# Kernel tuning notes

Hardware: AMD Instinct MI355X
Metric: run time of the kernel (lower is better)

## Reference

```python
import jax, jax.numpy as jnp
import numpy as np

C = 1.0                      # curvature
PHI = 3.1415926 * 0.3        # Cosine phase (bias=False path)
ALPHA = 0.2                  # LeakyReLU negative slope
A_PARA = 0.5                 # a_para_GATLayer
EPS = 4e-3                   # float32 ball-projection epsilon (standard HGCN)
MIN_NORM = 1e-15
NEG_INF = -9e15              # matches -9000000000000000.0 in source


def project(x, c):
    # clamp points to lie inside the Poincare ball of curvature c
    norm = jnp.maximum(jnp.linalg.norm(x, axis=-1, keepdims=True), MIN_NORM)
    maxnorm = (1.0 - EPS) / jnp.sqrt(c)
    return jnp.where(norm > maxnorm, x / norm * maxnorm, x)


def artanh(x):
    return jnp.arctanh(jnp.clip(x, -1.0 + 1e-7, 1.0 - 1e-7))


def logmap0(p, c):
    # log map at the origin of the Poincare ball
    sqrt_c = c ** 0.5
    p_norm = jnp.maximum(jnp.linalg.norm(p, axis=-1, keepdims=True), MIN_NORM)
    return artanh(sqrt_c * p_norm) / (sqrt_c * p_norm) * p


def setup_inputs() -> dict:
    key = jax.random.key(0)
    k1, k2, k3, k4 = jax.random.split(key, 4)
    N, FIN, FOUT = 8192, 512, 128
    h = jax.random.normal(k1, (N, FIN), dtype=jnp.float32)
    adj = jax.random.randint(k2, (N, N), 0, 2, dtype=jnp.int32)
    # xavier_uniform with gain=1.414
    lim_w = 1.414 * np.sqrt(6.0 / (FIN + FOUT))
    W = jax.random.uniform(k3, (FIN, FOUT), jnp.float32, -lim_w, lim_w)
    lim_a = 1.414 * np.sqrt(6.0 / (2 * FOUT + 1))
    a = jax.random.uniform(k4, (2 * FOUT, 1), jnp.float32, -lim_a, lim_a)
    return {"h": h, "adj": adj, "W": W, "a": a}


def reference(h, adj, W, a):
    fout = W.shape[1]
    Wh = h @ W                                   # [N, F_out]
    Wh1 = Wh @ a[:fout]                          # [N, 1] source score
    Wh2 = Wh @ a[fout:]                          # [N, 1] target score
    e = jax.nn.leaky_relu(Wh1 + Wh2.T, ALPHA)    # [N, N]
    e = jnp.where(adj > 0, e, NEG_INF)
    attention = jax.nn.softmax(e, axis=1)        # dropout p=0 (eval): identity
    h_prime = attention @ Wh                     # [N, F_out]
    h_prime = logmap0(project(h_prime, C), C)
    # concat=True branch: ELU + a_para * A*cos(x + phi), A=1 (data_dim=-1)
    return jax.nn.elu(h_prime) + A_PARA * jnp.cos(h_prime + PHI)
```

## Files before the change

kernel.cpp:

```cpp
#include <hip/hip_runtime.h>
#include <hip/hip_bf16.h>
#include <math.h>

typedef short short8 __attribute__((ext_vector_type(8)));
typedef float f32x4 __attribute__((ext_vector_type(4)));

static constexpr int N = 8192;
static constexpr int FIN = 512;
static constexpr int FOUT = 128;
static constexpr int NJC = 16;
static constexpr float PHI = 3.1415926f * 0.3f;
static constexpr float A_PARA = 0.5f;
static constexpr float EPS_BALL = 4e-3f;
static constexpr float L2E = 1.4426950408889634f;

__device__ __forceinline__ unsigned short f2b(float f) {
    union { float f; unsigned u; } v; v.f = f;
    unsigned r = v.u + 0x7fffu + ((v.u >> 16) & 1u);
    return (unsigned short)(r >> 16);
}

__device__ __forceinline__ short f2bn(float f) {
    __hip_bfloat16 h = __float2bfloat16(f);
    return *reinterpret_cast<short*>(&h);
}

__device__ __forceinline__ unsigned f2key(float x) {
    unsigned b = __float_as_uint(x);
    return (b & 0x80000000u) ? ~b : (b | 0x80000000u);
}
__device__ __forceinline__ float key2f(unsigned k) {
    unsigned b = (k & 0x80000000u) ? (k ^ 0x80000000u) : ~k;
    return __uint_as_float(b);
}

__device__ __forceinline__ short8 cvt8(float4 x0, float4 x1) {
    short8 r;
    r[0] = (short)f2b(x0.x); r[1] = (short)f2b(x0.y);
    r[2] = (short)f2b(x0.z); r[3] = (short)f2b(x0.w);
    r[4] = (short)f2b(x1.x); r[5] = (short)f2b(x1.y);
    r[6] = (short)f2b(x1.z); r[7] = (short)f2b(x1.w);
    return r;
}

__device__ __forceinline__ void cw(float* w, const int4 a, const float4 tv,
                                   float sA, float mA) {
    float z;
    z = sA + tv.x; w[0] = a.x > 0 ? __builtin_amdgcn_exp2f(fmaxf(z, 0.2f * z) - mA) : 0.f;
    z = sA + tv.y; w[1] = a.y > 0 ? __builtin_amdgcn_exp2f(fmaxf(z, 0.2f * z) - mA) : 0.f;
    z = sA + tv.z; w[2] = a.z > 0 ? __builtin_amdgcn_exp2f(fmaxf(z, 0.2f * z) - mA) : 0.f;
    z = sA + tv.w; w[3] = a.w > 0 ? __builtin_amdgcn_exp2f(fmaxf(z, 0.2f * z) - mA) : 0.f;
}

__global__ __launch_bounds__(256) void k0_wt(const float* __restrict__ W,
                                             unsigned short* __restrict__ Wt,
                                             unsigned* __restrict__ Tkey,
                                             float* __restrict__ denb) {
    __shared__ float sh[32][33];
    const int t = threadIdx.x;
    const int k0 = (blockIdx.x >> 2) * 32, c0 = (blockIdx.x & 3) * 32;
    {
        int r = t >> 3, c4 = (t & 7) * 4;
        float4 v = *(const float4*)(W + (size_t)(k0 + r) * FOUT + c0 + c4);
        sh[r][c4] = v.x; sh[r][c4 + 1] = v.y; sh[r][c4 + 2] = v.z; sh[r][c4 + 3] = v.w;
    }
    __syncthreads();
    int cc = t >> 3, k4 = (t & 7) * 4;
    ushort4 o;
    o.x = f2b(sh[k4][cc]); o.y = f2b(sh[k4 + 1][cc]);
    o.z = f2b(sh[k4 + 2][cc]); o.w = f2b(sh[k4 + 3][cc]);
    *(ushort4*)(Wt + (size_t)(c0 + cc) * FIN + k0 + k4) = o;
    if (blockIdx.x == 0) {
        if (t == 0) Tkey[0] = 0u;
        for (int i = t; i < N; i += 256) denb[i] = 0.f;
    }
}

__global__ __launch_bounds__(256) void k1_gemm(
    const float* __restrict__ h, const unsigned short* __restrict__ Wt,
    const float* __restrict__ a, unsigned short* __restrict__ whbt,
    float* __restrict__ s_out, float* __restrict__ t_out,
    unsigned* __restrict__ Tkey)
{
    __shared__ unsigned short hsb[2][32][72];
    __shared__ float sred[32][2], tred[32][2];
    const int t = threadIdx.x, lane = t & 63, wave = t >> 6;
    const int i0 = blockIdx.x * 32;
    const int wr = wave & 1, wc = wave >> 1;
    const int arow = lane & 15, g = lane >> 4;
    const int sr = t >> 3, sc = (t & 7) * 8;
    const float* hp = h + (size_t)(i0 + sr) * FIN + sc;

    float4 x0 = *(const float4*)hp, x1 = *(const float4*)(hp + 4);
    *(short8*)&hsb[0][sr][sc] = cvt8(x0, x1);
    __syncthreads();

    f32x4 acc[4];
    const f32x4 zz = {0.f, 0.f, 0.f, 0.f};
    #pragma unroll
    for (int cf = 0; cf < 4; ++cf) acc[cf] = zz;

    #pragma unroll 1
    for (int kt = 0; kt < 8; ++kt) {
        const int cur = kt & 1;
        float4 y0, y1;
        if (kt < 7) {
            y0 = *(const float4*)(hp + (kt + 1) * 64);
            y1 = *(const float4*)(hp + (kt + 1) * 64 + 4);
        }
        #pragma unroll
        for (int js = 0; js < 64; js += 32) {
            short8 af = *(const short8*)&hsb[cur][wr * 16 + arow][js + g * 8];
            #pragma unroll
            for (int cf = 0; cf < 4; ++cf) {
                const unsigned short* bp =
                    Wt + (size_t)(wc * 64 + cf * 16 + arow) * FIN + kt * 64 + js + g * 8;
                short8 bf = *(const short8*)bp;
                acc[cf] = __builtin_amdgcn_mfma_f32_16x16x32_bf16(af, bf, acc[cf], 0, 0, 0);
            }
        }
        if (kt < 7) {
            *(short8*)&hsb[cur ^ 1][sr][sc] = cvt8(y0, y1);
            __syncthreads();
        }
    }

    float a1v[4], a2v[4];
    #pragma unroll
    for (int cf = 0; cf < 4; ++cf) {
        int col = wc * 64 + cf * 16 + arow;
        a1v[cf] = a[col]; a2v[cf] = a[FOUT + col];
    }
    #pragma unroll
    for (int cf = 0; cf < 4; ++cf) {
        int col = wc * 64 + cf * 16 + arow;
        ushort4 o;
        o.x = f2b(acc[cf][0]); o.y = f2b(acc[cf][1]);
        o.z = f2b(acc[cf][2]); o.w = f2b(acc[cf][3]);
        *(ushort4*)(whbt + (size_t)col * N + i0 + wr * 16 + g * 4) = o;
    }
    #pragma unroll
    for (int q = 0; q < 4; ++q) {
        float sp = acc[0][q]*a1v[0] + acc[1][q]*a1v[1] + acc[2][q]*a1v[2] + acc[3][q]*a1v[3];
        float tp = acc[0][q]*a2v[0] + acc[1][q]*a2v[1] + acc[2][q]*a2v[2] + acc[3][q]*a2v[3];
        #pragma unroll
        for (int m = 1; m < 16; m <<= 1) {
            sp += __shfl_xor(sp, m, 16);
            tp += __shfl_xor(tp, m, 16);
        }
        if (arow == 0) {
            sred[wr * 16 + g * 4 + q][wc] = sp;
            tred[wr * 16 + g * 4 + q][wc] = tp;
        }
    }
    __syncthreads();
    if (t < 32) {
        float sp = (sred[t][0] + sred[t][1]) * L2E;
        float tp = (tred[t][0] + tred[t][1]) * L2E;
        s_out[i0 + t] = sp;
        t_out[i0 + t] = tp;
        float m = tp;
        #pragma unroll
        for (int d = 1; d < 32; d <<= 1) m = fmaxf(m, __shfl_xor(m, d, 32));
        if (t == 0) atomicMax(Tkey, f2key(m));
    }
}

__global__ __launch_bounds__(512, 4) void k3_attn(
    const int* __restrict__ adj, const unsigned short* __restrict__ whbt,
    const float* __restrict__ s_in, const float* __restrict__ t_in,
    const unsigned* __restrict__ Tkey,
    unsigned short* __restrict__ num_bf, float* __restrict__ num_f32,
    float* __restrict__ den_out, int slice_mode)
{
    __shared__ unsigned short bt[2][128][72];
    __shared__ float tl[512];
    const int t = threadIdx.x, lane = t & 63, wave = t >> 6;
    const int jc = blockIdx.x & (NJC - 1), it = blockIdx.x / NJC;
    const int i0 = it * 128, jbase = jc * (N / NJC);

    tl[t] = t_in[jbase + t];

    const int arow = lane & 15, g = lane >> 4;
    const int grow = i0 + wave * 16 + arow;
    const float sA = s_in[grow];
    const float Tv = key2f(Tkey[0]);
    const float zT = sA + Tv;
    const float mA = fmaxf(zT, 0.2f * zT);
    const int* adjrow = adj + (size_t)grow * N;
    const int srow = t >> 2, scol = (t & 3) * 16;
    const unsigned short* sbase = whbt + (size_t)srow * N + jbase + scol;

    f32x4 acc[8];
    const f32x4 zz = {0.f, 0.f, 0.f, 0.f};
    #pragma unroll
    for (int c = 0; c < 8; ++c) acc[c] = zz;
    float den = 0.f;

    short8 sr0 = *(const short8*)sbase;
    short8 sr1 = *(const short8*)(sbase + 8);
    int4 av0 = *(const int4*)(adjrow + jbase + g * 8);
    int4 av1 = *(const int4*)(adjrow + jbase + g * 8 + 4);
    int4 av2 = *(const int4*)(adjrow + jbase + 32 + g * 8);
    int4 av3 = *(const int4*)(adjrow + jbase + 32 + g * 8 + 4);
    *(short8*)&bt[0][srow][scol]     = sr0;
    *(short8*)&bt[0][srow][scol + 8] = sr1;
    __syncthreads();

    #pragma unroll 1
    for (int jt = 0; jt < 8; ++jt) {
        const int cur = jt & 1, jl = jt * 64;
        short8 n0, n1;
        if (jt < 7) {
            const unsigned short* p = sbase + (jt + 1) * 64;
            n0 = *(const short8*)p;
            n1 = *(const short8*)(p + 8);
        }
        int4 an0, an1, an2, an3;
        if (jt < 7) {
            const int* ap = adjrow + jbase + jl + 64;
            an0 = *(const int4*)(ap + g * 8);
            an1 = *(const int4*)(ap + g * 8 + 4);
            an2 = *(const int4*)(ap + 32 + g * 8);
            an3 = *(const int4*)(ap + 32 + g * 8 + 4);
        }
        float4 ta = *(const float4*)&tl[jl + g * 8];
        float4 tb = *(const float4*)&tl[jl + g * 8 + 4];
        float4 tc = *(const float4*)&tl[jl + 32 + g * 8];
        float4 td = *(const float4*)&tl[jl + 32 + g * 8 + 4];
        float w[16];
        cw(&w[0],  av0, ta, sA, mA);
        cw(&w[4],  av1, tb, sA, mA);
        cw(&w[8],  av2, tc, sA, mA);
        cw(&w[12], av3, td, sA, mA);
        #pragma unroll
        for (int e = 0; e < 16; ++e) den += w[e];
        short8 af0, af1;
        #pragma unroll
        for (int e = 0; e < 8; ++e) {
            af0[e] = f2bn(w[e]);
            af1[e] = f2bn(w[8 + e]);
        }
        #pragma unroll
        for (int c = 0; c < 8; ++c) {
            short8 bf = *(const short8*)&bt[cur][c * 16 + arow][g * 8];
            acc[c] = __builtin_amdgcn_mfma_f32_16x16x32_bf16(af0, bf, acc[c], 0, 0, 0);
        }
        #pragma unroll
        for (int c = 0; c < 8; ++c) {
            short8 bf = *(const short8*)&bt[cur][c * 16 + arow][32 + g * 8];
            acc[c] = __builtin_amdgcn_mfma_f32_16x16x32_bf16(af1, bf, acc[c], 0, 0, 0);
        }
        if (jt < 7) {
            *(short8*)&bt[cur ^ 1][srow][scol]     = n0;
            *(short8*)&bt[cur ^ 1][srow][scol + 8] = n1;
            av0 = an0; av1 = an1; av2 = an2; av3 = an3;
            __syncthreads();
        }
    }

    den += __shfl_xor(den, 16, 64);
    den += __shfl_xor(den, 32, 64);
    if (g == 0) atomicAdd(&den_out[grow], den);

    const int orow0 = i0 + wave * 16;
    if (slice_mode) {
        unsigned short* dst = num_bf + (size_t)jc * ((size_t)N * FOUT);
        #pragma unroll
        for (int c = 0; c < 8; ++c)
            #pragma unroll
            for (int q = 0; q < 4; ++q)
                dst[(size_t)(orow0 + g * 4 + q) * FOUT + c * 16 + arow] = f2b(acc[c][q]);
    } else {
        #pragma unroll
        for (int c = 0; c < 8; ++c)
            #pragma unroll
            for (int q = 0; q < 4; ++q)
                atomicAdd(&num_f32[(size_t)(orow0 + g * 4 + q) * FOUT + c * 16 + arow], acc[c][q]);
    }
}

__global__ __launch_bounds__(256) void k4_epi(
    const unsigned short* __restrict__ numb, const float* __restrict__ numf,
    const float* __restrict__ den, float* __restrict__ out, int bfmode)
{
    const int row = blockIdx.x * 16 + (threadIdx.x >> 4);
    const int col0 = (threadIdx.x & 15) * 8;
    const float inv = 1.0f / den[row];
    float v[8] = {};
    if (bfmode) {
        #pragma unroll 1
        for (int s5 = 0; s5 < NJC; ++s5) {
            short8 b = *(const short8*)(numb + (size_t)s5 * N * FOUT + (size_t)row * FOUT + col0);
            #pragma unroll
            for (int c = 0; c < 8; ++c)
                v[c] += __uint_as_float(((unsigned)(unsigned short)b[c]) << 16);
        }
    } else {
        #pragma unroll
        for (int c = 0; c < 8; ++c) v[c] = numf[(size_t)row * FOUT + col0 + c];
    }
    float ss = 0.f;
    #pragma unroll
    for (int c = 0; c < 8; ++c) { v[c] *= inv; ss += v[c] * v[c]; }
    #pragma unroll
    for (int m = 1; m < 16; m <<= 1) ss += __shfl_xor(ss, m, 16);
    float nrm = sqrtf(ss);
    const float maxn = 1.0f - EPS_BALL;
    float scale1 = nrm > maxn ? maxn / nrm : 1.0f;
    float pn = fminf(nrm, maxn);
    float fac;
    if (pn < 1e-6f) fac = scale1;
    else fac = scale1 * (0.5f * __logf((1.f + pn) / (1.f - pn))) / pn;
    float o[8];
    #pragma unroll
    for (int c = 0; c < 8; ++c) {
        float hv = v[c] * fac;
        float eluv = hv > 0.f ? hv : __expf(hv) - 1.f;
        o[c] = eluv + A_PARA * __cosf(hv + PHI);
    }
    float* op = out + (size_t)row * FOUT + col0;
    *(float4*)op = make_float4(o[0], o[1], o[2], o[3]);
    *(float4*)(op + 4) = make_float4(o[4], o[5], o[6], o[7]);
}

extern "C" void kernel_launch(void* const* d_in, const int* in_sizes, int n_in,
                              void* d_out, int out_size, void* d_ws, size_t ws_size,
                              hipStream_t stream) {
    const float* h   = (const float*)d_in[0];
    const int*   adj = (const int*)d_in[1];
    const float* W   = (const float*)d_in[2];
    const float* a   = (const float*)d_in[3];
    float* out = (float*)d_out;

    char* ws = (char*)d_ws;
    unsigned short* whbt = (unsigned short*)ws;
    size_t off = (size_t)N * FOUT * 2;
    unsigned short* Wt = (unsigned short*)(ws + off); off += (size_t)FOUT * FIN * 2;
    float* s  = (float*)(ws + off); off += (size_t)N * 4;
    float* tt = (float*)(ws + off); off += (size_t)N * 4;
    unsigned* Tkey = (unsigned*)(ws + off); off += 256;
    float* denb = (float*)(ws + off); off += (size_t)N * 4;
    const size_t slice_bytes = (size_t)N * FOUT * 2;
    const bool fast = ws_size >= off + (size_t)NJC * slice_bytes;
    unsigned short* numb = fast ? (unsigned short*)(ws + off) : nullptr;

    if (!fast) hipMemsetAsync(out, 0, (size_t)N * FOUT * 4, stream);

    k0_wt<<<64, 256, 0, stream>>>(W, Wt, Tkey, denb);
    k1_gemm<<<N / 32, 256, 0, stream>>>(h, Wt, a, whbt, s, tt, Tkey);
    k3_attn<<<(N / 128) * NJC, 512, 0, stream>>>(adj, whbt, s, tt, Tkey, numb, out, denb, fast ? 1 : 0);
    k4_epi<<<N / 16, 256, 0, stream>>>(numb, out, denb, out, fast ? 1 : 0);
}
```

Measured before the change: 102.2 us.

## Halve attention j-splits, deepen prefetch to two tiles, stage W in LDS

```diff
diff --git a/kernel.cpp b/kernel.cpp
--- a/kernel.cpp
+++ b/kernel.cpp
@@ -8,7 +8,7 @@
 static constexpr int N = 8192;
 static constexpr int FIN = 512;
 static constexpr int FOUT = 128;
-static constexpr int NJC = 16;
+static constexpr int NJC = 8;
 static constexpr float PHI = 3.1415926f * 0.3f;
 static constexpr float A_PARA = 0.5f;
 static constexpr float EPS_BALL = 4e-3f;
@@ -82,6 +82,7 @@
     float* __restrict__ s_out, float* __restrict__ t_out,
     unsigned* __restrict__ Tkey)
 {
+    __shared__ unsigned short wlds[128][520];
     __shared__ unsigned short hsb[2][32][72];
     __shared__ float sred[32][2], tred[32][2];
     const int t = threadIdx.x, lane = t & 63, wave = t >> 6;
@@ -91,6 +92,10 @@
     const int sr = t >> 3, sc = (t & 7) * 8;
     const float* hp = h + (size_t)(i0 + sr) * FIN + sc;
 
+    for (int idx = t; idx < (FOUT * FIN) / 8; idx += 256) {
+        const int row = idx >> 6, col = (idx & 63) * 8;
+        *(short8*)&wlds[row][col] = *(const short8*)(Wt + (size_t)row * FIN + col);
+    }
     float4 x0 = *(const float4*)hp, x1 = *(const float4*)(hp + 4);
     *(short8*)&hsb[0][sr][sc] = cvt8(x0, x1);
     __syncthreads();
@@ -113,9 +118,7 @@
             short8 af = *(const short8*)&hsb[cur][wr * 16 + arow][js + g * 8];
             #pragma unroll
             for (int cf = 0; cf < 4; ++cf) {
-                const unsigned short* bp =
-                    Wt + (size_t)(wc * 64 + cf * 16 + arow) * FIN + kt * 64 + js + g * 8;
-                short8 bf = *(const short8*)bp;
+                short8 bf = *(const short8*)&wlds[wc * 64 + cf * 16 + arow][kt * 64 + js + g * 8];
                 acc[cf] = __builtin_amdgcn_mfma_f32_16x16x32_bf16(af, bf, acc[cf], 0, 0, 0);
             }
         }
@@ -174,12 +177,13 @@
     float* __restrict__ den_out, int slice_mode)
 {
     __shared__ unsigned short bt[2][128][72];
-    __shared__ float tl[512];
+    __shared__ float tl[1024];
     const int t = threadIdx.x, lane = t & 63, wave = t >> 6;
     const int jc = blockIdx.x & (NJC - 1), it = blockIdx.x / NJC;
     const int i0 = it * 128, jbase = jc * (N / NJC);
 
     tl[t] = t_in[jbase + t];
+    tl[t + 512] = t_in[jbase + t + 512];
 
     const int arow = lane & 15, g = lane >> 4;
     const int grow = i0 + wave * 16 + arow;
@@ -197,28 +201,32 @@
     for (int c = 0; c < 8; ++c) acc[c] = zz;
     float den = 0.f;
 
-    short8 sr0 = *(const short8*)sbase;
-    short8 sr1 = *(const short8*)(sbase + 8);
+    short8 s00 = *(const short8*)sbase;
+    short8 s01 = *(const short8*)(sbase + 8);
+    short8 nc0 = *(const short8*)(sbase + 64);
+    short8 nc1 = *(const short8*)(sbase + 72);
     int4 av0 = *(const int4*)(adjrow + jbase + g * 8);
     int4 av1 = *(const int4*)(adjrow + jbase + g * 8 + 4);
     int4 av2 = *(const int4*)(adjrow + jbase + 32 + g * 8);
     int4 av3 = *(const int4*)(adjrow + jbase + 32 + g * 8 + 4);
-    *(short8*)&bt[0][srow][scol]     = sr0;
-    *(short8*)&bt[0][srow][scol + 8] = sr1;
+    *(short8*)&bt[0][srow][scol]     = s00;
+    *(short8*)&bt[0][srow][scol + 8] = s01;
     __syncthreads();
 
     #pragma unroll 1
-    for (int jt = 0; jt < 8; ++jt) {
+    for (int jt = 0; jt < 16; ++jt) {
         const int cur = jt & 1, jl = jt * 64;
-        short8 n0, n1;
-        if (jt < 7) {
-            const unsigned short* p = sbase + (jt + 1) * 64;
-            n0 = *(const short8*)p;
-            n1 = *(const short8*)(p + 8);
-        }
+        const int jt2 = (jt + 2 < 16) ? jt + 2 : 15;
+        short8 nn0, nn1;
+        {
+            const unsigned short* p = sbase + jt2 * 64;
+            nn0 = *(const short8*)p;
+            nn1 = *(const short8*)(p + 8);
+        }
+        const int jt1 = (jt + 1 < 16) ? jt + 1 : 15;
         int4 an0, an1, an2, an3;
-        if (jt < 7) {
-            const int* ap = adjrow + jbase + jl + 64;
+        {
+            const int* ap = adjrow + jbase + jt1 * 64;
             an0 = *(const int4*)(ap + g * 8);
             an1 = *(const int4*)(ap + g * 8 + 4);
             an2 = *(const int4*)(ap + 32 + g * 8);
@@ -251,9 +259,10 @@
             short8 bf = *(const short8*)&bt[cur][c * 16 + arow][32 + g * 8];
             acc[c] = __builtin_amdgcn_mfma_f32_16x16x32_bf16(af1, bf, acc[c], 0, 0, 0);
         }
-        if (jt < 7) {
-            *(short8*)&bt[cur ^ 1][srow][scol]     = n0;
-            *(short8*)&bt[cur ^ 1][srow][scol + 8] = n1;
+        if (jt < 15) {
+            *(short8*)&bt[cur ^ 1][srow][scol]     = nc0;
+            *(short8*)&bt[cur ^ 1][srow][scol + 8] = nc1;
+            nc0 = nn0; nc1 = nn1;
             av0 = an0; av1 = an1; av2 = an2; av3 = an3;
             __syncthreads();
         }
```

New measurement: 93.90 us (median of 3 runs). 1.09x faster.

## Stage full Wh slice and W into LDS once, deepen adjacency prefetch

Applied to the files above, without the earlier changes.

```diff
diff --git a/kernel.cpp b/kernel.cpp
--- a/kernel.cpp
+++ b/kernel.cpp
@@ -82,6 +82,7 @@
     float* __restrict__ s_out, float* __restrict__ t_out,
     unsigned* __restrict__ Tkey)
 {
+    __shared__ unsigned short wlds[128][520];
     __shared__ unsigned short hsb[2][32][72];
     __shared__ float sred[32][2], tred[32][2];
     const int t = threadIdx.x, lane = t & 63, wave = t >> 6;
@@ -91,6 +92,10 @@
     const int sr = t >> 3, sc = (t & 7) * 8;
     const float* hp = h + (size_t)(i0 + sr) * FIN + sc;
 
+    for (int idx = t; idx < (FOUT * FIN) / 8; idx += 256) {
+        const int row = idx >> 6, col = (idx & 63) * 8;
+        *(short8*)&wlds[row][col] = *(const short8*)(Wt + (size_t)row * FIN + col);
+    }
     float4 x0 = *(const float4*)hp, x1 = *(const float4*)(hp + 4);
     *(short8*)&hsb[0][sr][sc] = cvt8(x0, x1);
     __syncthreads();
@@ -113,9 +118,7 @@
             short8 af = *(const short8*)&hsb[cur][wr * 16 + arow][js + g * 8];
             #pragma unroll
             for (int cf = 0; cf < 4; ++cf) {
-                const unsigned short* bp =
-                    Wt + (size_t)(wc * 64 + cf * 16 + arow) * FIN + kt * 64 + js + g * 8;
-                short8 bf = *(const short8*)bp;
+                short8 bf = *(const short8*)&wlds[wc * 64 + cf * 16 + arow][kt * 64 + js + g * 8];
                 acc[cf] = __builtin_amdgcn_mfma_f32_16x16x32_bf16(af, bf, acc[cf], 0, 0, 0);
             }
         }
@@ -166,19 +169,23 @@
     }
 }
 
-__global__ __launch_bounds__(512, 4) void k3_attn(
+__global__ __launch_bounds__(512, 2) void k3_attn(
     const int* __restrict__ adj, const unsigned short* __restrict__ whbt,
     const float* __restrict__ s_in, const float* __restrict__ t_in,
     const unsigned* __restrict__ Tkey,
     unsigned short* __restrict__ num_bf, float* __restrict__ num_f32,
     float* __restrict__ den_out, int slice_mode)
 {
-    __shared__ unsigned short bt[2][128][72];
+    __shared__ unsigned short bt[128][520];
     __shared__ float tl[512];
     const int t = threadIdx.x, lane = t & 63, wave = t >> 6;
     const int jc = blockIdx.x & (NJC - 1), it = blockIdx.x / NJC;
     const int i0 = it * 128, jbase = jc * (N / NJC);
 
+    for (int idx = t; idx < (128 * 512) / 8; idx += 512) {
+        const int row = idx >> 6, col = (idx & 63) * 8;
+        *(short8*)&bt[row][col] = *(const short8*)(whbt + (size_t)row * N + jbase + col);
+    }
     tl[t] = t_in[jbase + t];
 
     const int arow = lane & 15, g = lane >> 4;
@@ -188,8 +195,6 @@
     const float zT = sA + Tv;
     const float mA = fmaxf(zT, 0.2f * zT);
     const int* adjrow = adj + (size_t)grow * N;
-    const int srow = t >> 2, scol = (t & 3) * 16;
-    const unsigned short* sbase = whbt + (size_t)srow * N + jbase + scol;
 
     f32x4 acc[8];
     const f32x4 zz = {0.f, 0.f, 0.f, 0.f};
@@ -197,67 +202,62 @@
     for (int c = 0; c < 8; ++c) acc[c] = zz;
     float den = 0.f;
 
-    short8 sr0 = *(const short8*)sbase;
-    short8 sr1 = *(const short8*)(sbase + 8);
-    int4 av0 = *(const int4*)(adjrow + jbase + g * 8);
-    int4 av1 = *(const int4*)(adjrow + jbase + g * 8 + 4);
-    int4 av2 = *(const int4*)(adjrow + jbase + 32 + g * 8);
-    int4 av3 = *(const int4*)(adjrow + jbase + 32 + g * 8 + 4);
-    *(short8*)&bt[0][srow][scol]     = sr0;
-    *(short8*)&bt[0][srow][scol + 8] = sr1;
+    int4 aA0 = *(const int4*)(adjrow + jbase + g * 8);
+    int4 aA1 = *(const int4*)(adjrow + jbase + g * 8 + 4);
+    int4 aA2 = *(const int4*)(adjrow + jbase + 32 + g * 8);
+    int4 aA3 = *(const int4*)(adjrow + jbase + 32 + g * 8 + 4);
+    int4 aB0 = *(const int4*)(adjrow + jbase + 64 + g * 8);
+    int4 aB1 = *(const int4*)(adjrow + jbase + 64 + g * 8 + 4);
+    int4 aB2 = *(const int4*)(adjrow + jbase + 96 + g * 8);
+    int4 aB3 = *(const int4*)(adjrow + jbase + 96 + g * 8 + 4);
+
     __syncthreads();
 
+#define K3_ITER(JT, U0, U1, U2, U3)                                            \
+    {                                                                          \
+        const int jl = (JT) * 64;                                              \
+        const int jn = ((JT) + 2 < 8) ? (JT) + 2 : 7;                          \
+        const int* ap = adjrow + jbase + jn * 64;                              \
+        int4 f0 = *(const int4*)(ap + g * 8);                                  \
+        int4 f1 = *(const int4*)(ap + g * 8 + 4);                              \
+        int4 f2 = *(const int4*)(ap + 32 + g * 8);                             \
+        int4 f3 = *(const int4*)(ap + 32 + g * 8 + 4);                         \
+        float4 ta = *(const float4*)&tl[jl + g * 8];                           \
+        float4 tb = *(const float4*)&tl[jl + g * 8 + 4];                       \
+        float4 tc = *(const float4*)&tl[jl + 32 + g * 8];                      \
+        float4 td = *(const float4*)&tl[jl + 32 + g * 8 + 4];                  \
+        float w[16];                                                           \
+        cw(&w[0],  U0, ta, sA, mA);                                            \
+        cw(&w[4],  U1, tb, sA, mA);                                            \
+        cw(&w[8],  U2, tc, sA, mA);                                            \
+        cw(&w[12], U3, td, sA, mA);                                            \
+        _Pragma("unroll")                                                      \
+        for (int e = 0; e < 16; ++e) den += w[e];                              \
+        short8 af0, af1;                                                       \
+        _Pragma("unroll")                                                      \
+        for (int e = 0; e < 8; ++e) {                                          \
+            af0[e] = f2bn(w[e]);                                               \
+            af1[e] = f2bn(w[8 + e]);                                           \
+        }                                                                      \
+        _Pragma("unroll")                                                      \
+        for (int c = 0; c < 8; ++c) {                                          \
+            short8 bf = *(const short8*)&bt[c * 16 + arow][jl + g * 8];        \
+            acc[c] = __builtin_amdgcn_mfma_f32_16x16x32_bf16(af0, bf, acc[c], 0, 0, 0); \
+        }                                                                      \
+        _Pragma("unroll")                                                      \
+        for (int c = 0; c < 8; ++c) {                                          \
+            short8 bf = *(const short8*)&bt[c * 16 + arow][jl + 32 + g * 8];   \
+            acc[c] = __builtin_amdgcn_mfma_f32_16x16x32_bf16(af1, bf, acc[c], 0, 0, 0); \
+        }                                                                      \
+        U0 = f0; U1 = f1; U2 = f2; U3 = f3;                                    \
+    }
+
     #pragma unroll 1
-    for (int jt = 0; jt < 8; ++jt) {
-        const int cur = jt & 1, jl = jt * 64;
-        short8 n0, n1;
-        if (jt < 7) {
-            const unsigned short* p = sbase + (jt + 1) * 64;
-            n0 = *(const short8*)p;
-            n1 = *(const short8*)(p + 8);
-        }
-        int4 an0, an1, an2, an3;
-        if (jt < 7) {
-            const int* ap = adjrow + jbase + jl + 64;
-            an0 = *(const int4*)(ap + g * 8);
-            an1 = *(const int4*)(ap + g * 8 + 4);
-            an2 = *(const int4*)(ap + 32 + g * 8);
-            an3 = *(const int4*)(ap + 32 + g * 8 + 4);
-        }
-        float4 ta = *(const float4*)&tl[jl + g * 8];
-        float4 tb = *(const float4*)&tl[jl + g * 8 + 4];
-        float4 tc = *(const float4*)&tl[jl + 32 + g * 8];
-        float4 td = *(const float4*)&tl[jl + 32 + g * 8 + 4];
-        float w[16];
-        cw(&w[0],  av0, ta, sA, mA);
-        cw(&w[4],  av1, tb, sA, mA);
-        cw(&w[8],  av2, tc, sA, mA);
-        cw(&w[12], av3, td, sA, mA);
-        #pragma unroll
-        for (int e = 0; e < 16; ++e) den += w[e];
-        short8 af0, af1;
-        #pragma unroll
-        for (int e = 0; e < 8; ++e) {
-            af0[e] = f2bn(w[e]);
-            af1[e] = f2bn(w[8 + e]);
-        }
-        #pragma unroll
-        for (int c = 0; c < 8; ++c) {
-            short8 bf = *(const short8*)&bt[cur][c * 16 + arow][g * 8];
-            acc[c] = __builtin_amdgcn_mfma_f32_16x16x32_bf16(af0, bf, acc[c], 0, 0, 0);
-        }
-        #pragma unroll
-        for (int c = 0; c < 8; ++c) {
-            short8 bf = *(const short8*)&bt[cur][c * 16 + arow][32 + g * 8];
-            acc[c] = __builtin_amdgcn_mfma_f32_16x16x32_bf16(af1, bf, acc[c], 0, 0, 0);
-        }
-        if (jt < 7) {
-            *(short8*)&bt[cur ^ 1][srow][scol]     = n0;
-            *(short8*)&bt[cur ^ 1][srow][scol + 8] = n1;
-            av0 = an0; av1 = an1; av2 = an2; av3 = an3;
-            __syncthreads();
-        }
-    }
+    for (int jp = 0; jp < 8; jp += 2) {
+        K3_ITER(jp,     aA0, aA1, aA2, aA3);
+        K3_ITER(jp + 1, aB0, aB1, aB2, aB3);
+    }
+#undef K3_ITER
 
     den += __shfl_xor(den, 16, 64);
     den += __shfl_xor(den, 32, 64);
```

After: 122.1 us. 1.19x slower.
